# Performance work log

Hardware: AMD Instinct MI355X
Metric: run time of the kernel (lower is better)

## Reference

```python
import jax, jax.numpy as jnp
import numpy as np

N = 8192   # decoder nodes (batch*seq)
M = 8192   # encoder memory nodes
D = 512    # d_model (layer.size)
H = 8      # attention heads
DK = D // H
DFF = 2048 # feed-forward hidden
E = 262144 # edges per attention graph (avg in-degree 32)
EPS = 1e-6


def _ln(x, g, b):
    # LayerNorm over last dim (annotated-transformer style, eps=1e-6)
    mu = x.mean(-1, keepdims=True)
    var = ((x - mu) ** 2).mean(-1, keepdims=True)
    return (x - mu) * jax.lax.rsqrt(var + EPS) * g + b


def _heads(t):
    return t.reshape(-1, H, DK)


def _attend(q, k, v, src, dst, n_dst):
    # per-edge score = exp(clip(k_src . q_dst / sqrt(dk))), scatter-sum to dst
    score = jnp.einsum('ehd,ehd->eh', k[src], q[dst]) * np.float32(1.0 / np.sqrt(DK))
    score = jnp.exp(jnp.clip(score, -10.0, 10.0))
    wv = jax.ops.segment_sum(score[:, :, None] * v[src], dst, num_segments=n_dst)  # [n_dst,H,DK]
    z = jax.ops.segment_sum(score, dst, num_segments=n_dst)                         # [n_dst,H]
    return (wv / z[:, :, None]).reshape(n_dst, D)


def setup_inputs() -> dict:
    key = jax.random.key(0)
    ks = jax.random.split(key, 16)
    f = lambda k, shape, s: jax.random.normal(k, shape, dtype=jnp.float32) * np.float32(s)
    inp = {
        'x': f(ks[0], (N, D), 1.0),
        'mem': f(ks[1], (M, D), 1.0),
        'ln0_g': jnp.ones((D,), jnp.float32), 'ln0_b': jnp.zeros((D,), jnp.float32),
        'ln1_g': jnp.ones((D,), jnp.float32), 'ln1_b': jnp.zeros((D,), jnp.float32),
        'ln2_g': jnp.ones((D,), jnp.float32), 'ln2_b': jnp.zeros((D,), jnp.float32),
        'Wq': f(ks[2], (D, D), D ** -0.5), 'bq': jnp.zeros((D,), jnp.float32),
        'Wk': f(ks[3], (D, D), D ** -0.5), 'bk': jnp.zeros((D,), jnp.float32),
        'Wv': f(ks[4], (D, D), D ** -0.5), 'bv': jnp.zeros((D,), jnp.float32),
        'Wo': f(ks[5], (D, D), D ** -0.5), 'bo': jnp.zeros((D,), jnp.float32),
        'W1': f(ks[6], (D, DFF), D ** -0.5), 'b1': jnp.zeros((DFF,), jnp.float32),
        'W2': f(ks[7], (DFF, D), DFF ** -0.5), 'b2': jnp.zeros((D,), jnp.float32),
        'src_self': jax.random.randint(ks[8], (E,), 0, N),
        'dst_self': jax.random.randint(ks[9], (E,), 0, N),
        'src_cross': jax.random.randint(ks[10], (E,), 0, M),
        'dst_cross': jax.random.randint(ks[11], (E,), 0, N),
    }
    return inp


def reference(x, mem, ln0_g, ln0_b, ln1_g, ln1_b, ln2_g, ln2_b,
              Wq, bq, Wk, bk, Wv, bv, Wo, bo, W1, b1, W2, b2,
              src_self, dst_self, src_cross, dst_cross):
    # l=0: self-attention. pre_func('qkv',0): norm then qkv projections.
    h = _ln(x, ln0_g, ln0_b)
    q = _heads(h @ Wq + bq)
    k = _heads(h @ Wk + bk)
    v = _heads(h @ Wv + bv)
    # post_func(0): o = W_o(wv/z); x = x + dropout(o) (eval: identity)
    o = _attend(q, k, v, src_self, dst_self, N) @ Wo + bo
    x = x + o
    # l=1: cross-attention. pre_func('q',1): norm on decoder nodes;
    # pre_func('kv'): NO norm on memory nodes (norm_x = x branch).
    h = _ln(x, ln1_g, ln1_b)
    q = _heads(h @ Wq + bq)
    km = _heads(mem @ Wk + bk)
    vm = _heads(mem @ Wv + bv)
    o = _attend(q, km, vm, src_cross, dst_cross, N) @ Wo + bo
    x = x + o
    # post_func(1): feed-forward sublayer x + dropout(FF(LN(x)))
    h = _ln(x, ln2_g, ln2_b)
    x = x + (jax.nn.relu(h @ W1 + b1) @ W2 + b2)
    return x
```

## Files before the change

kernel.cpp:

```cpp
#include <hip/hip_runtime.h>
#include <cstdint>
#include <cstddef>

#define DEV __device__ __forceinline__

typedef __attribute__((ext_vector_type(4))) float f32x4;
typedef __attribute__((ext_vector_type(2))) float f32x2;
typedef __attribute__((ext_vector_type(4))) unsigned int u32x4;
typedef __attribute__((ext_vector_type(2))) unsigned int u32x2;
typedef unsigned short ushort_t;

constexpr int NN  = 8192;
constexpr int MMM = 8192;
constexpr int DD  = 512;
constexpr int DFF = 2048;

DEV unsigned short f2bf(float f) {
  unsigned int u = __builtin_bit_cast(unsigned int, f);
  u += 0x7fffu + ((u >> 16) & 1u);
  return (unsigned short)(u >> 16);
}
DEV float bflo(unsigned int u) { return __builtin_bit_cast(float, u << 16); }
DEV float bfhi(unsigned int u) { return __builtin_bit_cast(float, u & 0xffff0000u); }
DEV unsigned char f2fp8(float f) {
  int p = __builtin_amdgcn_cvt_pk_fp8_f32(f, f, 0, false);
  return (unsigned char)(p & 0xff);
}

DEV void gload_lds16(const void* g, void* l) {
  __builtin_amdgcn_global_load_lds((__attribute__((address_space(1))) void*)g,
                                   (__attribute__((address_space(3))) void*)l,
                                   16, 0, 0);
}

DEV void xcd_rc(int l, int gx, int gy, int& row, int& col) {
  const int xcd = l & 7;
  const int idx = l >> 3;
  const int rpx = gx >> 3;
  row = xcd * rpx + idx / gy;
  col = idx % gy;
}

__global__ void transw_kernel(const float* __restrict__ in, ushort_t* __restrict__ out,
                              int R, int C) {
  __shared__ float t[32][33];
  const int x0 = blockIdx.x * 32, y0 = blockIdx.y * 32;
  const int tx = threadIdx.x, ty = threadIdx.y;
#pragma unroll
  for (int i = 0; i < 4; ++i)
    t[ty + i * 8][tx] = in[(long)(y0 + ty + i * 8) * C + x0 + tx];
  __syncthreads();
#pragma unroll
  for (int i = 0; i < 4; ++i)
    out[(long)(x0 + ty + i * 8) * R + y0 + tx] = f2bf(t[tx][ty + i * 8]);
}

struct TW4 {
  const float* in0; const float* in1; const float* in2; const float* in3;
  ushort_t* o0; ushort_t* o1; ushort_t* o2; ushort_t* o3;
};
__global__ void transw4_kernel(TW4 p) {
  const float* in; ushort_t* out;
  switch (blockIdx.z) {
    case 0:  in = p.in0; out = p.o0; break;
    case 1:  in = p.in1; out = p.o1; break;
    case 2:  in = p.in2; out = p.o2; break;
    default: in = p.in3; out = p.o3; break;
  }
  __shared__ float t[32][33];
  const int x0 = blockIdx.x * 32, y0 = blockIdx.y * 32;
  const int tx = threadIdx.x, ty = threadIdx.y;
#pragma unroll
  for (int i = 0; i < 4; ++i)
    t[ty + i * 8][tx] = in[(long)(y0 + ty + i * 8) * 512 + x0 + tx];
  __syncthreads();
#pragma unroll
  for (int i = 0; i < 4; ++i)
    out[(long)(x0 + ty + i * 8) * 512 + y0 + tx] = f2bf(t[tx][ty + i * 8]);
}

__global__ void tobf_kernel(const float* __restrict__ in, ushort_t* __restrict__ out, int n4) {
  int i = blockIdx.x * blockDim.x + threadIdx.x;
  if (i >= n4) return;
  f32x4 v = ((const f32x4*)in)[i];
  u32x2 o;
  o[0] = (unsigned)f2bf(v[0]) | ((unsigned)f2bf(v[1]) << 16);
  o[1] = (unsigned)f2bf(v[2]) | ((unsigned)f2bf(v[3]) << 16);
  ((u32x2*)out)[i] = o;
}

__global__ void biascat_kernel(const float* __restrict__ bq, const float* __restrict__ bk,
                               const float* __restrict__ bv, float* __restrict__ o) {
  const int i = blockIdx.x * blockDim.x + threadIdx.x;
  if (i >= 1536) return;
  o[i] = (i < 512) ? bq[i] : ((i < 1024) ? bk[i - 512] : bv[i - 1024]);
}

__global__ __launch_bounds__(256)
void ln_kernel(const float* __restrict__ x, const float* __restrict__ g,
               const float* __restrict__ b, ushort_t* __restrict__ out) {
  const int row  = blockIdx.x * 4 + (threadIdx.x >> 6);
  const int lane = threadIdx.x & 63;
  const float* xr = x + (long)row * DD + lane * 8;
  float v[8];
  *(f32x4*)&v[0] = *(const f32x4*)&xr[0];
  *(f32x4*)&v[4] = *(const f32x4*)&xr[4];
  float s = 0.f, sq = 0.f;
#pragma unroll
  for (int i = 0; i < 8; ++i) { s += v[i]; sq += v[i] * v[i]; }
#pragma unroll
  for (int o = 1; o < 64; o <<= 1) { s += __shfl_xor(s, o); sq += __shfl_xor(sq, o); }
  const float mu   = s * (1.f / 512.f);
  const float var  = sq * (1.f / 512.f) - mu * mu;
  const float rstd = rsqrtf(var + 1e-6f);
  const float* gp = g + lane * 8;
  const float* bp = b + lane * 8;
  u32x4 o8;
#pragma unroll
  for (int u = 0; u < 4; ++u) {
    unsigned int lo = f2bf((v[2 * u]     - mu) * rstd * gp[2 * u]     + bp[2 * u]);
    unsigned int hi = f2bf((v[2 * u + 1] - mu) * rstd * gp[2 * u + 1] + bp[2 * u + 1]);
    o8[u] = lo | (hi << 16);
  }
  *(u32x4*)(out + (long)row * DD + lane * 8) = o8;
}


template <int EPI>
__global__ __launch_bounds__(256, 4)
void gemm_kernel(const ushort_t* __restrict__ A, const ushort_t* __restrict__ Bt,
                 const float* __restrict__ bias, const float* res,
                 float* outF, ushort_t* outB, unsigned char* out8, int M, int N, int K) {
  __shared__ __align__(16) ushort_t sA[128 * 64];
  __shared__ __align__(16) ushort_t sB[128 * 64];
  const int tid  = threadIdx.x;
  const int lane = tid & 63;
  const int w    = tid >> 6;
  const int wr   = w >> 1, wc = w & 1;
  int brc, bcc;
  xcd_rc(blockIdx.x, M >> 7, N >> 7, brc, bcc);
  const long brow = (long)brc * 128;
  const long bcol = (long)bcc * 128;
  const int r16 = lane & 15;
  const int cq  = lane >> 4;
  f32x4 acc[4][4] = {};

  for (int k0 = 0; k0 < K; k0 += 64) {
    __syncthreads();
#pragma unroll
    for (int i = 0; i < 4; ++i) {
      const int c   = i * 256 + tid;
      const int wb  = i * 256 + (tid & ~63);
      const int row = c >> 3;
      const int col = ((c & 7) ^ (row & 7)) << 3;
      gload_lds16(A  + (brow + row) * (long)K + k0 + col, &sA[(long)wb * 8]);
      gload_lds16(Bt + (bcol + row) * (long)K + k0 + col, &sB[(long)wb * 8]);
    }
    __syncthreads();
#pragma unroll
    for (int kkc = 0; kkc < 8; kkc += 4) {
      u32x4 af[4], bfr[4];
#pragma unroll
      for (int i = 0; i < 4; ++i) {
        const int row = wr * 64 + i * 16 + r16;
        af[i] = *(const u32x4*)&sA[row * 64 + (((kkc + cq) ^ (row & 7)) << 3)];
      }
#pragma unroll
      for (int j = 0; j < 4; ++j) {
        const int row = wc * 64 + j * 16 + r16;
        bfr[j] = *(const u32x4*)&sB[row * 64 + (((kkc + cq) ^ (row & 7)) << 3)];
      }
#pragma unroll
      for (int i = 0; i < 4; ++i)
#pragma unroll
        for (int j = 0; j < 4; ++j)
          asm("v_mfma_f32_16x16x32_bf16 %0, %1, %2, %0"
              : "+v"(acc[i][j]) : "v"(af[i]), "v"(bfr[j]));
    }
  }
  asm volatile("s_nop 7\n\ts_nop 7\n\ts_nop 7" ::);

  const long orow = brow + wr * 64;
  const long ocol = bcol + wc * 64;
#pragma unroll
  for (int j = 0; j < 4; ++j) {
    const long c  = ocol + j * 16 + r16;
    const float bv = bias[c];
#pragma unroll
    for (int i = 0; i < 4; ++i) {
      const long r0 = orow + i * 16 + ((lane >> 4) << 2);
#pragma unroll
      for (int r = 0; r < 4; ++r) {
        float v = acc[i][j][r] + bv;
        const long row = r0 + r;
        if (EPI == 0)      outB[row * (long)N + c] = f2bf(v);
        else if (EPI == 1) outB[row * (long)N + c] = f2bf(fmaxf(v, 0.f));
        else if (EPI == 2) outF[row * (long)N + c] = v + res[row * (long)N + c];
        else if (EPI == 3) out8[row * (long)N + c] = f2fp8(v);
        else {
          if (c < 512) outB[row * 512 + c] = f2bf(v);
          else         out8[row * 1024 + (c - 512)] = f2fp8(v);
        }
      }
    }
  }
}

template <int EPI>
__global__ __launch_bounds__(256, 8)
void gemm64b_kernel(const ushort_t* __restrict__ A, const ushort_t* __restrict__ Bt,
                    const float* __restrict__ bias, const float* res,
                    float* outF, ushort_t* outB, unsigned char* out8, int M, int N, int K) {
  __shared__ __align__(16) ushort_t sA[64 * 64];
  __shared__ __align__(16) ushort_t sB[64 * 64];
  const int tid  = threadIdx.x;
  const int lane = tid & 63;
  const int w    = tid >> 6;
  const int wr   = w >> 1, wc = w & 1;
  int brc, bcc;
  xcd_rc(blockIdx.x, M >> 6, N >> 6, brc, bcc);
  const long brow = (long)brc * 64;
  const long bcol = (long)bcc * 64;
  const int r16 = lane & 15;
  const int cq  = lane >> 4;
  f32x4 acc[2][2] = {};

  for (int k0 = 0; k0 < K; k0 += 64) {
    __syncthreads();
#pragma unroll
    for (int i = 0; i < 2; ++i) {
      const int c   = i * 256 + tid;
      const int wb  = i * 256 + (tid & ~63);
      const int row = c >> 3;
      const int col = ((c & 7) ^ (row & 7)) << 3;
      gload_lds16(A  + (brow + row) * (long)K + k0 + col, &sA[(long)wb * 8]);
      gload_lds16(Bt + (bcol + row) * (long)K + k0 + col, &sB[(long)wb * 8]);
    }
    __syncthreads();
#pragma unroll
    for (int kkc = 0; kkc < 8; kkc += 4) {
      u32x4 af[2], bfr[2];
#pragma unroll
      for (int i = 0; i < 2; ++i) {
        const int row = wr * 32 + i * 16 + r16;
        af[i] = *(const u32x4*)&sA[row * 64 + (((kkc + cq) ^ (row & 7)) << 3)];
      }
#pragma unroll
      for (int j = 0; j < 2; ++j) {
        const int row = wc * 32 + j * 16 + r16;
        bfr[j] = *(const u32x4*)&sB[row * 64 + (((kkc + cq) ^ (row & 7)) << 3)];
      }
#pragma unroll
      for (int i = 0; i < 2; ++i)
#pragma unroll
        for (int j = 0; j < 2; ++j)
          asm("v_mfma_f32_16x16x32_bf16 %0, %1, %2, %0"
              : "+v"(acc[i][j]) : "v"(af[i]), "v"(bfr[j]));
    }
  }
  asm volatile("s_nop 7\n\ts_nop 7\n\ts_nop 7" ::);

  const long orow = brow + wr * 32;
  const long ocol = bcol + wc * 32;
#pragma unroll
  for (int j = 0; j < 2; ++j) {
    const long c  = ocol + j * 16 + r16;
    const float bv = bias[c];
#pragma unroll
    for (int i = 0; i < 2; ++i) {
      const long r0 = orow + i * 16 + ((lane >> 4) << 2);
#pragma unroll
      for (int r = 0; r < 4; ++r) {
        float v = acc[i][j][r] + bv;
        const long row = r0 + r;
        if (EPI == 0)      outB[row * (long)N + c] = f2bf(v);
        else if (EPI == 1) outB[row * (long)N + c] = f2bf(fmaxf(v, 0.f));
        else if (EPI == 2) outF[row * (long)N + c] = v + res[row * (long)N + c];
        else               out8[row * (long)N + c] = f2fp8(v);
      }
    }
  }
}

__global__ void zero_kernel(int* p, int n) {
  int i = blockIdx.x * blockDim.x + threadIdx.x;
  if (i < n) p[i] = 0;
}
__global__ void hist2_kernel(const int* __restrict__ d0, const int* __restrict__ d1,
                             int* __restrict__ counts2, int E) {
  const int* d = blockIdx.y ? d1 : d0;
  int* c = counts2 + blockIdx.y * 8192;
  for (int e = blockIdx.x * blockDim.x + threadIdx.x; e < E; e += gridDim.x * blockDim.x)
    atomicAdd(&c[d[e]], 1);
}
template <int PER, int BINS>
__global__ void scan_kernel(const int* __restrict__ countsN, int* __restrict__ rowstartN,
                            int* __restrict__ cursorN) {
  const int* counts = countsN + blockIdx.x * BINS;
  int* rowstart = rowstartN + blockIdx.x * (BINS + 1);
  int* cursor   = cursorN + blockIdx.x * BINS;
  __shared__ int part[256];
  const int t = threadIdx.x;
  int loc[PER];
  int s = 0;
  const int base = t * PER;
#pragma unroll
  for (int i = 0; i < PER; ++i) { loc[i] = counts[base + i]; s += loc[i]; }
  part[t] = s;
  __syncthreads();
  for (int off = 1; off < 256; off <<= 1) {
    int v2 = (t >= off) ? part[t - off] : 0;
    __syncthreads();
    part[t] += v2;
    __syncthreads();
  }
  int run = part[t] - s;
#pragma unroll
  for (int i = 0; i < PER; ++i) { rowstart[base + i] = run; cursor[base + i] = run; run += loc[i]; }
  if (t == 255) rowstart[BINS] = run;
}
__global__ void scatterD_kernel(const int* __restrict__ s0, const int* __restrict__ d0,
                                const int* __restrict__ s1, const int* __restrict__ d1,
                                int* __restrict__ cursorD2,
                                int* __restrict__ o0, int* __restrict__ o1, int E) {
  const int* s = blockIdx.y ? s1 : s0;
  const int* d = blockIdx.y ? d1 : d0;
  int* cur = cursorD2 + blockIdx.y * 8192;
  int* o = blockIdx.y ? o1 : o0;
  for (int e = blockIdx.x * blockDim.x + threadIdx.x; e < E; e += gridDim.x * blockDim.x) {
    const int p = atomicAdd(&cur[d[e]], 1);
    o[p] = s[e];
  }
}

#define ATT_LOADI(SD, EB)                                                   \
  _Pragma("unroll") for (int jj = 0; jj < 4; ++jj) {                        \
    int e_ = (EB) + jj;                                                     \
    SD[jj] = srcs[e_ < e1 ? e_ : e1 - 1];                                   \
  }
#define ATT_LOADG(KD, VD, SD)                                               \
  _Pragma("unroll") for (int jj = 0; jj < 4; ++jj) {                        \
    const unsigned char* p_ = kvb + (long)SD[jj] * 1024 + boff;             \
    KD[jj] = *(const u32x2*)p_;                                             \
    VD[jj] = *(const u32x2*)(p_ + 512);                                     \
  }
#define ATT_EDGE(KF, VF, VALID)                                             \
  {                                                                         \
    f32x2 d2_ = {0.f, 0.f};                                                 \
    d2_ += (f32x2)__builtin_amdgcn_cvt_pk_f32_fp8((KF)[0], false) * q2[0];  \
    d2_ += (f32x2)__builtin_amdgcn_cvt_pk_f32_fp8((KF)[0], true)  * q2[1];  \
    d2_ += (f32x2)__builtin_amdgcn_cvt_pk_f32_fp8((KF)[1], false) * q2[2];  \
    d2_ += (f32x2)__builtin_amdgcn_cvt_pk_f32_fp8((KF)[1], true)  * q2[3];  \
    float dot_ = d2_[0] + d2_[1];                                           \
    dot_ += __shfl_xor(dot_, 1);                                            \
    dot_ += __shfl_xor(dot_, 2);                                            \
    dot_ += __shfl_xor(dot_, 4);                                            \
    float sc_ = __expf(fminf(fmaxf(dot_ * 0.125f, -10.f), 10.f));           \
    sc_ = (VALID) ? sc_ : 0.f;                                              \
    z += sc_;                                                               \
    const f32x2 s2_ = {sc_, sc_};                                           \
    av[0] += s2_ * (f32x2)__builtin_amdgcn_cvt_pk_f32_fp8((VF)[0], false);  \
    av[1] += s2_ * (f32x2)__builtin_amdgcn_cvt_pk_f32_fp8((VF)[0], true);   \
    av[2] += s2_ * (f32x2)__builtin_amdgcn_cvt_pk_f32_fp8((VF)[1], false);  \
    av[3] += s2_ * (f32x2)__builtin_amdgcn_cvt_pk_f32_fp8((VF)[1], true);   \
  }
#define ATT_GROUP(GB, K4, V4)                                               \
  _Pragma("unroll") for (int jj = 0; jj < 4; ++jj) {                        \
    ATT_EDGE(K4[jj], V4[jj], ((GB) + jj < n))                               \
  }

__global__ __launch_bounds__(256)
void attend_kernel(const int* __restrict__ rowstart, const int* __restrict__ srcs,
                   const ushort_t* __restrict__ qb,
                   const unsigned char* __restrict__ kvb,
                   ushort_t* __restrict__ ob) {
  const int d    = blockIdx.x * 4 + (threadIdx.x >> 6);
  const int lane = threadIdx.x & 63;
  const int boff = lane * 8;
  const int e0 = rowstart[d], e1 = rowstart[d + 1];
  const int n  = e1 - e0;
  const u32x4 qv = *(const u32x4*)(qb + (long)d * DD + lane * 8);
  f32x2 q2[4];
#pragma unroll
  for (int u = 0; u < 4; ++u) q2[u] = f32x2{bflo(qv[u]), bfhi(qv[u])};
  f32x2 av[4] = {};
  float z = 0.f;
  if (n > 0) {
    int sA4[4], sB4[4];
    u32x2 kA4[4], vA4[4], kB4[4], vB4[4];
    ATT_LOADI(sA4, e0);
    ATT_LOADI(sB4, e0 + 4);
    ATT_LOADG(kA4, vA4, sA4);
    const int ng = (n + 3) >> 2;
    const int NG = (ng + 1) & ~1;
    for (int g = 0; g < NG; g += 2) {
      ATT_LOADG(kB4, vB4, sB4);
      ATT_LOADI(sA4, e0 + (g + 2) * 4);
      ATT_GROUP(g * 4, kA4, vA4)
      ATT_LOADG(kA4, vA4, sA4);
      ATT_LOADI(sB4, e0 + (g + 3) * 4);
      ATT_GROUP((g + 1) * 4, kB4, vB4)
    }
  }
  const float inv = 1.f / z;
  u32x4 o;
#pragma unroll
  for (int u = 0; u < 4; ++u)
    o[u] = (unsigned)f2bf(av[u][0] * inv) | ((unsigned)f2bf(av[u][1] * inv) << 16);
  *(u32x4*)(ob + (long)d * DD + lane * 8) = o;
}

extern "C" void kernel_launch(void* const* d_in, const int* in_sizes, int n_in,
                              void* d_out, int out_size, void* d_ws, size_t ws_size,
                              hipStream_t stream) {
  const float* x    = (const float*)d_in[0];
  const float* mem  = (const float*)d_in[1];
  const float* ln0g = (const float*)d_in[2];  const float* ln0b = (const float*)d_in[3];
  const float* ln1g = (const float*)d_in[4];  const float* ln1b = (const float*)d_in[5];
  const float* ln2g = (const float*)d_in[6];  const float* ln2b = (const float*)d_in[7];
  const float* Wq = (const float*)d_in[8];   const float* bq = (const float*)d_in[9];
  const float* Wk = (const float*)d_in[10];  const float* bk = (const float*)d_in[11];
  const float* Wv = (const float*)d_in[12];  const float* bv = (const float*)d_in[13];
  const float* Wo = (const float*)d_in[14];  const float* bo = (const float*)d_in[15];
  const float* W1 = (const float*)d_in[16];  const float* b1 = (const float*)d_in[17];
  const float* W2 = (const float*)d_in[18];  const float* b2 = (const float*)d_in[19];
  const int* src_self  = (const int*)d_in[20];
  const int* dst_self  = (const int*)d_in[21];
  const int* src_cross = (const int*)d_in[22];
  const int* dst_cross = (const int*)d_in[23];
  const int E = in_sizes[20];
  float* out = (float*)d_out;

  char* wsp = (char*)d_ws;
  auto alloc = [&](size_t bytes) {
    char* p = wsp;
    wsp += (bytes + 255) & ~(size_t)255;
    return p;
  };
  ushort_t* Wqkv_t = (ushort_t*)alloc((size_t)1536 * 512 * 2);
  ushort_t* Wo_t   = (ushort_t*)alloc((size_t)512 * 512 * 2);
  ushort_t* W1_t   = (ushort_t*)alloc((size_t)DFF * DD * 2);
  ushort_t* W2_t   = (ushort_t*)alloc((size_t)DD * DFF * 2);
  float*    bqkv   = (float*)alloc(1536 * 4);
  ushort_t* h_bf   = (ushort_t*)alloc((size_t)NN * DD * 2);
  ushort_t* mem_bf = (ushort_t*)alloc((size_t)MMM * DD * 2);
  ushort_t* q_bf   = (ushort_t*)alloc((size_t)NN * DD * 2);
  unsigned char* kvf8 = (unsigned char*)alloc((size_t)NN * 1024);
  ushort_t* attn_bf= (ushort_t*)alloc((size_t)NN * DD * 2);
  ushort_t* ffh_bf = (ushort_t*)alloc((size_t)NN * DFF * 2);
  int* countsD   = (int*)alloc(2 * 8192 * 4);
  int* rowstartD2= (int*)alloc(2 * 8193 * 4);
  int* cursorD2  = (int*)alloc(2 * 8192 * 4);
  int* srcsA     = (int*)alloc((size_t)E * 4);
  int* srcsB     = (int*)alloc((size_t)E * 4);

  const dim3 B256(256);

  TW4 tw{Wq, Wk, Wv, Wo, Wqkv_t, Wqkv_t + 512 * 512, Wqkv_t + 1024 * 512, Wo_t};
  transw4_kernel<<<dim3(16, 16, 4), dim3(32, 8), 0, stream>>>(tw);
  transw_kernel<<<dim3(64, 16), dim3(32, 8), 0, stream>>>(W1, W1_t, DD, DFF);
  transw_kernel<<<dim3(16, 64), dim3(32, 8), 0, stream>>>(W2, W2_t, DFF, DD);
  biascat_kernel<<<dim3(6), B256, 0, stream>>>(bq, bk, bv, bqkv);
  tobf_kernel<<<dim3(MMM * DD / 4 / 256), B256, 0, stream>>>(mem, mem_bf, MMM * DD / 4);
  zero_kernel<<<dim3(64), B256, 0, stream>>>(countsD, 2 * 8192);
  hist2_kernel<<<dim3(256, 2), B256, 0, stream>>>(dst_self, dst_cross, countsD, E);
  scan_kernel<32, 8192><<<dim3(2), B256, 0, stream>>>(countsD, rowstartD2, cursorD2);
  scatterD_kernel<<<dim3(256, 2), B256, 0, stream>>>(src_self, dst_self, src_cross, dst_cross,
                                                     cursorD2, srcsA, srcsB, E);

  auto gemm = [&](int mode, const ushort_t* Ap, const ushort_t* Btp, const float* biasp,
                  const float* resp, float* oF, ushort_t* oB, unsigned char* o8,
                  int M_, int N_, int K_) {
    if (N_ <= 1024) {
      dim3 g((M_ / 64) * (N_ / 64));
      if (mode == 0)
        gemm64b_kernel<0><<<g, B256, 0, stream>>>(Ap, Btp, biasp, resp, oF, oB, o8, M_, N_, K_);
      else if (mode == 1)
        gemm64b_kernel<1><<<g, B256, 0, stream>>>(Ap, Btp, biasp, resp, oF, oB, o8, M_, N_, K_);
      else if (mode == 2)
        gemm64b_kernel<2><<<g, B256, 0, stream>>>(Ap, Btp, biasp, resp, oF, oB, o8, M_, N_, K_);
      else
        gemm64b_kernel<3><<<g, B256, 0, stream>>>(Ap, Btp, biasp, resp, oF, oB, o8, M_, N_, K_);
    } else {
      dim3 g((M_ / 128) * (N_ / 128));
      if (mode == 0)
        gemm_kernel<0><<<g, B256, 0, stream>>>(Ap, Btp, biasp, resp, oF, oB, o8, M_, N_, K_);
      else if (mode == 1)
        gemm_kernel<1><<<g, B256, 0, stream>>>(Ap, Btp, biasp, resp, oF, oB, o8, M_, N_, K_);
      else if (mode == 2)
        gemm_kernel<2><<<g, B256, 0, stream>>>(Ap, Btp, biasp, resp, oF, oB, o8, M_, N_, K_);
      else if (mode == 3)
        gemm_kernel<3><<<g, B256, 0, stream>>>(Ap, Btp, biasp, resp, oF, oB, o8, M_, N_, K_);
      else
        gemm_kernel<4><<<g, B256, 0, stream>>>(Ap, Btp, biasp, resp, oF, oB, o8, M_, N_, K_);
    }
  };

  ln_kernel<<<dim3(NN / 4), B256, 0, stream>>>(x, ln0g, ln0b, h_bf);
  gemm(4, h_bf, Wqkv_t, bqkv, nullptr, nullptr, q_bf, kvf8, NN, 1536, DD);
  attend_kernel<<<dim3(NN / 4), B256, 0, stream>>>(rowstartD2, srcsA, q_bf, kvf8, attn_bf);
  gemm(2, attn_bf, Wo_t, bo, x, out, nullptr, nullptr, NN, DD, DD);

  ln_kernel<<<dim3(NN / 4), B256, 0, stream>>>(out, ln1g, ln1b, h_bf);
  gemm(0, h_bf, Wqkv_t, bqkv, nullptr, nullptr, q_bf, nullptr, NN, 512, DD);
  gemm(3, mem_bf, Wqkv_t + 512 * 512, bqkv + 512, nullptr, nullptr, nullptr, kvf8,
       MMM, 1024, DD);
  attend_kernel<<<dim3(NN / 4), B256, 0, stream>>>(rowstartD2 + 8193, srcsB, q_bf, kvf8, attn_bf);
  gemm(2, attn_bf, Wo_t, bo, out, out, nullptr, nullptr, NN, DD, DD);

  ln_kernel<<<dim3(NN / 4), B256, 0, stream>>>(out, ln2g, ln2b, h_bf);
  gemm(1, h_bf, W1_t, b1, nullptr, nullptr, ffh_bf, nullptr, NN, DFF, DD);
  gemm(2, ffh_bf, W2_t, b2, out, out, nullptr, nullptr, NN, DD, DFF);

  (void)n_in; (void)out_size; (void)ws_size; (void)in_sizes;
}
```

Before: 283.4 us.

## Split fp8 K/V cache into head-half planes with interleaved K/V for attention

The K/V projection epilogue now writes fp8 K and V into two half-head planes (heads 0-3 and 4-7), with each 8-byte K chunk followed by its matching V chunk. The attention kernel is replaced by a variant that processes one half of the heads per launch with two destination nodes per wavefront. Each lane now issues one 16-byte gather per edge instead of two 8-byte ones, and each pass touches only a 4 MB plane, which is meant to improve cache locality of the random gathers. In exchange the attention runs as two launches, the edge lists are re-read, the lanes of the two nodes in a wave are imbalanced because both loop up to the larger degree, and the epilogue stores become scattered byte writes.

```diff
diff --git a/kernel.cpp b/kernel.cpp
--- a/kernel.cpp
+++ b/kernel.cpp
@@ -25,6 +25,13 @@
 DEV unsigned char f2fp8(float f) {
   int p = __builtin_amdgcn_cvt_pk_fp8_f32(f, f, 0, false);
   return (unsigned char)(p & 0xff);
+}
+
+DEV void store_kv(unsigned char* kv2, long node, int cc , float val) {
+  int h, off;
+  if (cc < 512) { h = cc >> 8; const int r = cc & 255; off = ((r >> 3) << 4) + (r & 7); }
+  else { const int cv = cc - 512; h = cv >> 8; const int r = cv & 255; off = ((r >> 3) << 4) + 8 + (r & 7); }
+  kv2[((long)h * 8192 + node) * 512 + off] = f2fp8(val);
 }
 
 DEV void gload_lds16(const void* g, void* l) {
@@ -196,10 +203,10 @@
         if (EPI == 0)      outB[row * (long)N + c] = f2bf(v);
         else if (EPI == 1) outB[row * (long)N + c] = f2bf(fmaxf(v, 0.f));
         else if (EPI == 2) outF[row * (long)N + c] = v + res[row * (long)N + c];
-        else if (EPI == 3) out8[row * (long)N + c] = f2fp8(v);
+        else if (EPI == 3) store_kv(out8, row, (int)c, v);
         else {
           if (c < 512) outB[row * 512 + c] = f2bf(v);
-          else         out8[row * 1024 + (c - 512)] = f2fp8(v);
+          else         store_kv(out8, row, (int)c - 512, v);
         }
       }
     }
@@ -276,7 +283,7 @@
         if (EPI == 0)      outB[row * (long)N + c] = f2bf(v);
         else if (EPI == 1) outB[row * (long)N + c] = f2bf(fmaxf(v, 0.f));
         else if (EPI == 2) outF[row * (long)N + c] = v + res[row * (long)N + c];
-        else               out8[row * (long)N + c] = f2fp8(v);
+        else               store_kv(out8, row, (int)c, v);
       }
     }
   }
@@ -327,30 +334,27 @@
   const int* d = blockIdx.y ? d1 : d0;
   int* cur = cursorD2 + blockIdx.y * 8192;
   int* o = blockIdx.y ? o1 : o0;
-  for (int e = blockIdx.x * blockDim.x + threadIdx.x; e < E; e += gridDim.x * blockDim.x) {
+  for (int e = blockIdx.x * blockDim.x + threadIdx.x; e += 0, e < E; e += gridDim.x * blockDim.x) {
     const int p = atomicAdd(&cur[d[e]], 1);
     o[p] = s[e];
   }
 }
 
-#define ATT_LOADI(SD, EB)                                                   \
+#define AT2_LOADI(SD, EB)                                                   \
   _Pragma("unroll") for (int jj = 0; jj < 4; ++jj) {                        \
     int e_ = (EB) + jj;                                                     \
     SD[jj] = srcs[e_ < e1 ? e_ : e1 - 1];                                   \
   }
-#define ATT_LOADG(KD, VD, SD)                                               \
-  _Pragma("unroll") for (int jj = 0; jj < 4; ++jj) {                        \
-    const unsigned char* p_ = kvb + (long)SD[jj] * 1024 + boff;             \
-    KD[jj] = *(const u32x2*)p_;                                             \
-    VD[jj] = *(const u32x2*)(p_ + 512);                                     \
-  }
-#define ATT_EDGE(KF, VF, VALID)                                             \
+#define AT2_LOADG(KV, SD)                                                   \
+  _Pragma("unroll") for (int jj = 0; jj < 4; ++jj)                          \
+    KV[jj] = *(const u32x4*)(kvb + (long)SD[jj] * 512 + boff);
+#define AT2_EDGE(KV, VALID)                                                 \
   {                                                                         \
     f32x2 d2_ = {0.f, 0.f};                                                 \
-    d2_ += (f32x2)__builtin_amdgcn_cvt_pk_f32_fp8((KF)[0], false) * q2[0];  \
-    d2_ += (f32x2)__builtin_amdgcn_cvt_pk_f32_fp8((KF)[0], true)  * q2[1];  \
-    d2_ += (f32x2)__builtin_amdgcn_cvt_pk_f32_fp8((KF)[1], false) * q2[2];  \
-    d2_ += (f32x2)__builtin_amdgcn_cvt_pk_f32_fp8((KF)[1], true)  * q2[3];  \
+    d2_ += (f32x2)__builtin_amdgcn_cvt_pk_f32_fp8((KV)[0], false) * q2[0];  \
+    d2_ += (f32x2)__builtin_amdgcn_cvt_pk_f32_fp8((KV)[0], true)  * q2[1];  \
+    d2_ += (f32x2)__builtin_amdgcn_cvt_pk_f32_fp8((KV)[1], false) * q2[2];  \
+    d2_ += (f32x2)__builtin_amdgcn_cvt_pk_f32_fp8((KV)[1], true)  * q2[3];  \
     float dot_ = d2_[0] + d2_[1];                                           \
     dot_ += __shfl_xor(dot_, 1);                                            \
     dot_ += __shfl_xor(dot_, 2);                                            \
@@ -359,47 +363,51 @@
     sc_ = (VALID) ? sc_ : 0.f;                                              \
     z += sc_;                                                               \
     const f32x2 s2_ = {sc_, sc_};                                           \
-    av[0] += s2_ * (f32x2)__builtin_amdgcn_cvt_pk_f32_fp8((VF)[0], false);  \
-    av[1] += s2_ * (f32x2)__builtin_amdgcn_cvt_pk_f32_fp8((VF)[0], true);   \
-    av[2] += s2_ * (f32x2)__builtin_amdgcn_cvt_pk_f32_fp8((VF)[1], false);  \
-    av[3] += s2_ * (f32x2)__builtin_amdgcn_cvt_pk_f32_fp8((VF)[1], true);   \
-  }
-#define ATT_GROUP(GB, K4, V4)                                               \
+    av[0] += s2_ * (f32x2)__builtin_amdgcn_cvt_pk_f32_fp8((KV)[2], false);  \
+    av[1] += s2_ * (f32x2)__builtin_amdgcn_cvt_pk_f32_fp8((KV)[2], true);   \
+    av[2] += s2_ * (f32x2)__builtin_amdgcn_cvt_pk_f32_fp8((KV)[3], false);  \
+    av[3] += s2_ * (f32x2)__builtin_amdgcn_cvt_pk_f32_fp8((KV)[3], true);   \
+  }
+#define AT2_GROUP(GB, KV4)                                                  \
   _Pragma("unroll") for (int jj = 0; jj < 4; ++jj) {                        \
-    ATT_EDGE(K4[jj], V4[jj], ((GB) + jj < n))                               \
+    AT2_EDGE(KV4[jj], ((GB) + jj < n))                                      \
   }
 
 __global__ __launch_bounds__(256)
-void attend_kernel(const int* __restrict__ rowstart, const int* __restrict__ srcs,
-                   const ushort_t* __restrict__ qb,
-                   const unsigned char* __restrict__ kvb,
-                   ushort_t* __restrict__ ob) {
-  const int d    = blockIdx.x * 4 + (threadIdx.x >> 6);
+void attend2_kernel(const int* __restrict__ rowstart, const int* __restrict__ srcs,
+                    const ushort_t* __restrict__ qb,
+                    const unsigned char* __restrict__ kvb,
+                    ushort_t* __restrict__ ob, int hoff) {
+  const int wid  = blockIdx.x * 4 + (threadIdx.x >> 6);
   const int lane = threadIdx.x & 63;
-  const int boff = lane * 8;
+  const int l32  = lane & 31;
+  const int d    = 2 * wid + (lane >> 5);
+  const int boff = l32 * 16;
   const int e0 = rowstart[d], e1 = rowstart[d + 1];
   const int n  = e1 - e0;
-  const u32x4 qv = *(const u32x4*)(qb + (long)d * DD + lane * 8);
+  int nmax = n;
+  nmax = max(nmax, __shfl_xor(nmax, 32));
+  const u32x4 qv = *(const u32x4*)(qb + (long)d * DD + hoff + l32 * 8);
   f32x2 q2[4];
 #pragma unroll
   for (int u = 0; u < 4; ++u) q2[u] = f32x2{bflo(qv[u]), bfhi(qv[u])};
   f32x2 av[4] = {};
   float z = 0.f;
-  if (n > 0) {
+  if (nmax > 0) {
     int sA4[4], sB4[4];
-    u32x2 kA4[4], vA4[4], kB4[4], vB4[4];
-    ATT_LOADI(sA4, e0);
-    ATT_LOADI(sB4, e0 + 4);
-    ATT_LOADG(kA4, vA4, sA4);
-    const int ng = (n + 3) >> 2;
+    u32x4 kvA[4], kvB[4];
+    AT2_LOADI(sA4, e0);
+    AT2_LOADI(sB4, e0 + 4);
+    AT2_LOADG(kvA, sA4);
+    const int ng = (nmax + 3) >> 2;
     const int NG = (ng + 1) & ~1;
     for (int g = 0; g < NG; g += 2) {
-      ATT_LOADG(kB4, vB4, sB4);
-      ATT_LOADI(sA4, e0 + (g + 2) * 4);
-      ATT_GROUP(g * 4, kA4, vA4)
-      ATT_LOADG(kA4, vA4, sA4);
-      ATT_LOADI(sB4, e0 + (g + 3) * 4);
-      ATT_GROUP((g + 1) * 4, kB4, vB4)
+      AT2_LOADG(kvB, sB4);
+      AT2_LOADI(sA4, e0 + (g + 2) * 4);
+      AT2_GROUP(g * 4, kvA)
+      AT2_LOADG(kvA, sA4);
+      AT2_LOADI(sB4, e0 + (g + 3) * 4);
+      AT2_GROUP((g + 1) * 4, kvB)
     }
   }
   const float inv = 1.f / z;
@@ -407,7 +415,7 @@
 #pragma unroll
   for (int u = 0; u < 4; ++u)
     o[u] = (unsigned)f2bf(av[u][0] * inv) | ((unsigned)f2bf(av[u][1] * inv) << 16);
-  *(u32x4*)(ob + (long)d * DD + lane * 8) = o;
+  *(u32x4*)(ob + (long)d * DD + hoff + l32 * 8) = o;
 }
 
 extern "C" void kernel_launch(void* const* d_in, const int* in_sizes, int n_in,
@@ -445,7 +453,7 @@
   ushort_t* h_bf   = (ushort_t*)alloc((size_t)NN * DD * 2);
   ushort_t* mem_bf = (ushort_t*)alloc((size_t)MMM * DD * 2);
   ushort_t* q_bf   = (ushort_t*)alloc((size_t)NN * DD * 2);
-  unsigned char* kvf8 = (unsigned char*)alloc((size_t)NN * 1024);
+  unsigned char* kv2 = (unsigned char*)alloc((size_t)2 * NN * 512);
   ushort_t* attn_bf= (ushort_t*)alloc((size_t)NN * DD * 2);
   ushort_t* ffh_bf = (ushort_t*)alloc((size_t)NN * DFF * 2);
   int* countsD   = (int*)alloc(2 * 8192 * 4);
@@ -495,17 +503,22 @@
         gemm_kernel<4><<<g, B256, 0, stream>>>(Ap, Btp, biasp, resp, oF, oB, o8, M_, N_, K_);
     }
   };
+  auto attend = [&](const int* rs, const int* sc) {
+    attend2_kernel<<<dim3(1024), B256, 0, stream>>>(rs, sc, q_bf, kv2, attn_bf, 0);
+    attend2_kernel<<<dim3(1024), B256, 0, stream>>>(rs, sc, q_bf,
+                                                    kv2 + (size_t)NN * 512, attn_bf, 256);
+  };
 
   ln_kernel<<<dim3(NN / 4), B256, 0, stream>>>(x, ln0g, ln0b, h_bf);
-  gemm(4, h_bf, Wqkv_t, bqkv, nullptr, nullptr, q_bf, kvf8, NN, 1536, DD);
-  attend_kernel<<<dim3(NN / 4), B256, 0, stream>>>(rowstartD2, srcsA, q_bf, kvf8, attn_bf);
+  gemm(4, h_bf, Wqkv_t, bqkv, nullptr, nullptr, q_bf, kv2, NN, 1536, DD);
+  attend(rowstartD2, srcsA);
   gemm(2, attn_bf, Wo_t, bo, x, out, nullptr, nullptr, NN, DD, DD);
 
   ln_kernel<<<dim3(NN / 4), B256, 0, stream>>>(out, ln1g, ln1b, h_bf);
   gemm(0, h_bf, Wqkv_t, bqkv, nullptr, nullptr, q_bf, nullptr, NN, 512, DD);
-  gemm(3, mem_bf, Wqkv_t + 512 * 512, bqkv + 512, nullptr, nullptr, nullptr, kvf8,
+  gemm(3, mem_bf, Wqkv_t + 512 * 512, bqkv + 512, nullptr, nullptr, nullptr, kv2,
        MMM, 1024, DD);
-  attend_kernel<<<dim3(NN / 4), B256, 0, stream>>>(rowstartD2 + 8193, srcsB, q_bf, kvf8, attn_bf);
+  attend(rowstartD2 + 8193, srcsB);
   gemm(2, attn_bf, Wo_t, bo, out, out, nullptr, nullptr, NN, DD, DD);
 
   ln_kernel<<<dim3(NN / 4), B256, 0, stream>>>(out, ln2g, ln2b, h_bf);
```

Result: slower. 292.9 us (+3.4%).
